# Performance work log

Hardware: AMD Instinct MI355X
Metric: run time of the kernel (lower is better)

The kernel has to match this reference:

```python
import jax, jax.numpy as jnp
import numpy as np

TAU = 0.1
EPS = 1e-8  # torch CosineSimilarity eps


def _neg_indices(B):
    # static (numpy) column indices of the non-masked (negative) entries per row
    N = 2 * B
    mask = ~(np.eye(N, dtype=bool)
             | np.eye(N, k=B, dtype=bool)
             | np.eye(N, k=-B, dtype=bool))
    return np.where(mask)[1].reshape(N, N - 2)  # [2B, 2B-2]


def setup_inputs() -> dict:
    key = jax.random.key(0)
    k1, k2 = jax.random.split(key)
    zis = jax.random.normal(k1, (4096, 128), dtype=jnp.float32)
    zjs = jax.random.normal(k2, (4096, 128), dtype=jnp.float32)
    return {"zis": zis, "zjs": zjs}


def reference(zis, zjs):
    B = zis.shape[0]
    N = 2 * B
    reps = jnp.concatenate([zjs, zis], axis=0)  # [2B, D]
    # cosine similarity via normalize + GEMM
    norm = jnp.linalg.norm(reps, axis=-1, keepdims=True)
    rn = reps / jnp.maximum(norm, EPS)
    sim = rn @ rn.T  # [2B, 2B]

    l_pos = jnp.diagonal(sim, offset=B)   # [B]
    r_pos = jnp.diagonal(sim, offset=-B)  # [B]
    positives = jnp.concatenate([l_pos, r_pos])[:, None]  # [2B, 1]

    neg_idx = jnp.asarray(_neg_indices(B))  # static [2B, 2B-2]
    negatives = jnp.take_along_axis(sim, neg_idx, axis=1)  # [2B, 2B-2]

    logits = jnp.concatenate([positives, negatives], axis=1) / TAU  # [2B, 2B-1]
    logp = jax.nn.log_softmax(logits, axis=-1)
    # labels are all zeros; CrossEntropyLoss(reduction='sum')
    CE = -jnp.sum(logp[:, 0])
    # pt = mean over full [2B, 2B-1] of onehot * softmax = sum softmax[:,0] / (2B*(2B-1))
    pt = jnp.sum(jnp.exp(logp[:, 0])) / (N * (N - 1))
    epsilon = float(B)
    loss = CE / N + epsilon * (1.0 / B - pt)
    return loss
```

## Files before the change

kernel.cpp:

```cpp
#include <hip/hip_runtime.h>
#include <hip/hip_bf16.h>

#define BSZ 4096
#define NSZ 8192
#define DD  128
#define TILE 128
#define GROUPS 8
#define TPB 8

typedef __attribute__((ext_vector_type(8))) short bf16x8;
typedef __attribute__((ext_vector_type(4))) float f32x4;

typedef __attribute__((address_space(3))) unsigned int lds_u32;
typedef const __attribute__((address_space(1))) unsigned int glb_u32;

__global__ __launch_bounds__(256)
void norm_kernel(const float* __restrict__ zis,
                 const float* __restrict__ zjs,
                 __hip_bfloat16* __restrict__ rn) {
    const int row  = blockIdx.x * 4 + (threadIdx.x >> 6);
    const int lane = threadIdx.x & 63;
    const float* src = (row < BSZ) ? (zjs + (size_t)row * DD)
                                   : (zis + (size_t)(row - BSZ) * DD);
    float2 v = *(const float2*)(src + lane * 2);
    float ss = v.x * v.x + v.y * v.y;
    #pragma unroll
    for (int off = 32; off; off >>= 1) ss += __shfl_xor(ss, off);
    float inv = 1.0f / fmaxf(sqrtf(ss), 1e-8f);
    __hip_bfloat16 a = __float2bfloat16(v.x * inv);
    __hip_bfloat16 b = __float2bfloat16(v.y * inv);
    ushort2 pk;
    pk.x = *(const ushort*)&a;
    pk.y = *(const ushort*)&b;
    *(ushort2*)(rn + (size_t)row * DD + lane * 2) = pk;
}

__global__ __launch_bounds__(512)
void sim_lse_kernel(const __hip_bfloat16* __restrict__ rn,
                    float* __restrict__ partials,
                    float* __restrict__ pos) {
    __shared__ ushort Bt[2][TILE * DD];

    const int g   = blockIdx.x;
    const int bi  = blockIdx.y;
    const int tid = threadIdx.x;
    const int wid  = tid >> 6;
    const int lane = tid & 63;
    const int l15  = lane & 15;
    const int kg   = lane >> 4;
    const int wm   = wid >> 1;
    const int wn   = wid & 1;

    const char* abase = (const char*)rn + (size_t)(bi * TILE + wm * 32 + l15) * 256;
    bf16x8 af[2][4];
    #pragma unroll
    for (int mf = 0; mf < 2; ++mf)
        #pragma unroll
        for (int kk = 0; kk < 4; ++kk)
            af[mf][kk] = *(const bf16x8*)(abase + mf * 16 * 256 + kk * 64 + kg * 16);

    {
        const char* gbase = (const char*)rn + (size_t)(g * TPB) * TILE * 256;
        #pragma unroll
        for (int j = 0; j < 4; ++j) {
            int cs  = (wid * 4 + j) * 64 + lane;
            int gsc = cs ^ ((cs >> 4) & 7);
            __builtin_amdgcn_global_load_lds((glb_u32*)(gbase + (size_t)gsc * 16),
                                             (lds_u32*)(&Bt[0][0] + (wid * 4 + j) * 512),
                                             16, 0, 0);
        }
    }
    __syncthreads();

    float rsum[2][4] = {};
    const int bjp = (bi + 32) & 63;
    const int nfd = (wm & 1) * 2;
    const bool wdiag = (wn == (wm >> 1));

    for (int t = 0; t < TPB; ++t) {
        const int bj = g * TPB + t;

        if (t + 1 < TPB) {
            const char* gbase = (const char*)rn + (size_t)(bj + 1) * TILE * 256;
            ushort* dst = &Bt[(t + 1) & 1][0];
            #pragma unroll
            for (int j = 0; j < 4; ++j) {
                int cs  = (wid * 4 + j) * 64 + lane;
                int gsc = cs ^ ((cs >> 4) & 7);
                __builtin_amdgcn_global_load_lds((glb_u32*)(gbase + (size_t)gsc * 16),
                                                 (lds_u32*)(dst + (wid * 4 + j) * 512),
                                                 16, 0, 0);
            }
        }

        f32x4 acc[2][4] = {};
        const char* Bb = (const char*)&Bt[t & 1][0];
        #pragma unroll
        for (int kk = 0; kk < 4; ++kk) {
            const int kb = kk * 64 + kg * 16;
            bf16x8 bfr[4];
            #pragma unroll
            for (int nf = 0; nf < 4; ++nf) {
                int cR = wn * 64 + nf * 16 + l15;
                int o = cR * 256 + kb;
                bfr[nf] = *(const bf16x8*)(Bb + (o ^ ((cR & 7) << 4)));
            }
            #pragma unroll
            for (int mf = 0; mf < 2; ++mf)
                #pragma unroll
                for (int nf = 0; nf < 4; ++nf)
                    acc[mf][nf] = __builtin_amdgcn_mfma_f32_16x16x32_bf16(
                        af[mf][kk], bfr[nf], acc[mf][nf], 0, 0, 0);
        }

        const bool dglb = (bj == bi)  && wdiag;
        const bool pglb = (bj == bjp) && wdiag;
        #pragma unroll
        for (int mf = 0; mf < 2; ++mf) {
            #pragma unroll
            for (int nf = 0; nf < 4; ++nf) {
                #pragma unroll
                for (int reg = 0; reg < 4; ++reg) {
                    float s = acc[mf][nf][reg];
                    bool hit = (nf == nfd + mf) && (kg * 4 + reg == l15);
                    if (pglb && hit)
                        pos[bi * TILE + wm * 32 + mf * 16 + l15] = s;
                    float p = __expf(s * 10.0f);
                    if (dglb && hit) p = 0.0f;
                    rsum[mf][reg] += p;
                }
            }
        }

        __syncthreads();
    }

    #pragma unroll
    for (int mf = 0; mf < 2; ++mf)
        #pragma unroll
        for (int reg = 0; reg < 4; ++reg) {
            float v = rsum[mf][reg];
            v += __shfl_xor(v, 1);
            v += __shfl_xor(v, 2);
            v += __shfl_xor(v, 4);
            v += __shfl_xor(v, 8);
            if (l15 == 0)
                partials[(size_t)(g * 2 + wn) * NSZ
                         + bi * TILE + wm * 32 + mf * 16 + kg * 4 + reg] = v;
        }
}

__global__ __launch_bounds__(1024)
void reduce_kernel(const float* __restrict__ partials,
                   const float* __restrict__ pos,
                   float* __restrict__ out) {
    int tid = threadIdx.x;
    int base = tid * 8;
    float se[8] = {0.f, 0.f, 0.f, 0.f, 0.f, 0.f, 0.f, 0.f};
    #pragma unroll
    for (int gr = 0; gr < 2 * GROUPS; ++gr) {
        const float* p = partials + (size_t)gr * NSZ + base;
        float4 a = *(const float4*)(p);
        float4 b = *(const float4*)(p + 4);
        se[0] += a.x; se[1] += a.y; se[2] += a.z; se[3] += a.w;
        se[4] += b.x; se[5] += b.y; se[6] += b.z; se[7] += b.w;
    }
    float ce = 0.f, pt = 0.f;
    #pragma unroll
    for (int h = 0; h < 2; ++h) {
        float4 p4 = *(const float4*)(pos + base + h * 4);
        const float* pp = (const float*)&p4;
        #pragma unroll
        for (int q = 0; q < 4; ++q) {
            float s = se[h * 4 + q];
            ce += __logf(s) - pp[q] * 10.0f;
            pt += __expf(pp[q] * 10.0f) / s;
        }
    }
    #pragma unroll
    for (int off = 32; off; off >>= 1) {
        ce += __shfl_xor(ce, off);
        pt += __shfl_xor(pt, off);
    }
    __shared__ float lce[16], lpt[16];
    if ((tid & 63) == 0) { lce[tid >> 6] = ce; lpt[tid >> 6] = pt; }
    __syncthreads();
    if (tid == 0) {
        float CE = 0.f, PT = 0.f;
        #pragma unroll
        for (int w = 0; w < 16; ++w) { CE += lce[w]; PT += lpt[w]; }
        float loss = CE / (float)NSZ + 1.0f
                   - PT * ((float)BSZ / ((float)NSZ * (float)(NSZ - 1)));
        out[0] = loss;
    }
}

extern "C" void kernel_launch(void* const* d_in, const int* in_sizes, int n_in,
                              void* d_out, int out_size, void* d_ws, size_t ws_size,
                              hipStream_t stream) {
    const float* zis = (const float*)d_in[0];
    const float* zjs = (const float*)d_in[1];
    float* out = (float*)d_out;

    char* ws = (char*)d_ws;
    __hip_bfloat16* rn = (__hip_bfloat16*)ws;
    float* partials = (float*)(ws + 2 * 1024 * 1024);
    float* pos      = (float*)(ws + 2 * 1024 * 1024 + 512 * 1024);

    norm_kernel<<<NSZ / 4, 256, 0, stream>>>(zis, zjs, rn);

    dim3 grid(GROUPS, 64);
    sim_lse_kernel<<<grid, 512, 0, stream>>>(rn, partials, pos);

    reduce_kernel<<<1, 1024, 0, stream>>>(partials, pos, out);
}
```

Before: 46.22 us.

## Stage A tile in LDS and single-buffer B to raise occupancy

The A fragments were held in registers for the whole kernel. They are now staged once into LDS and re-read every iteration. The B double buffer is replaced with a single buffer that is loaded after compute, with a second barrier per tile. A launch-bounds occupancy hint of 4 is added. The aim is to cut register pressure and allow more resident blocks, at the cost of extra LDS reads and losing the overlap of the global load with compute.

```diff
diff --git a/kernel.cpp b/kernel.cpp
--- a/kernel.cpp
+++ b/kernel.cpp
@@ -35,11 +35,12 @@
     *(ushort2*)(rn + (size_t)row * DD + lane * 2) = pk;
 }
 
-__global__ __launch_bounds__(512)
+__global__ __launch_bounds__(512, 4)
 void sim_lse_kernel(const __hip_bfloat16* __restrict__ rn,
                     float* __restrict__ partials,
                     float* __restrict__ pos) {
-    __shared__ ushort Bt[2][TILE * DD];
+    __shared__ ushort As[TILE * DD];
+    __shared__ ushort Bs[TILE * DD];
 
     const int g   = blockIdx.x;
     const int bi  = blockIdx.y;
@@ -51,22 +52,18 @@
     const int wm   = wid >> 1;
     const int wn   = wid & 1;
 
-    const char* abase = (const char*)rn + (size_t)(bi * TILE + wm * 32 + l15) * 256;
-    bf16x8 af[2][4];
-    #pragma unroll
-    for (int mf = 0; mf < 2; ++mf)
-        #pragma unroll
-        for (int kk = 0; kk < 4; ++kk)
-            af[mf][kk] = *(const bf16x8*)(abase + mf * 16 * 256 + kk * 64 + kg * 16);
-
     {
-        const char* gbase = (const char*)rn + (size_t)(g * TPB) * TILE * 256;
+        const char* ga = (const char*)rn + (size_t)bi * TILE * 256;
+        const char* gb = (const char*)rn + (size_t)(g * TPB) * TILE * 256;
         #pragma unroll
         for (int j = 0; j < 4; ++j) {
             int cs  = (wid * 4 + j) * 64 + lane;
             int gsc = cs ^ ((cs >> 4) & 7);
-            __builtin_amdgcn_global_load_lds((glb_u32*)(gbase + (size_t)gsc * 16),
-                                             (lds_u32*)(&Bt[0][0] + (wid * 4 + j) * 512),
+            __builtin_amdgcn_global_load_lds((glb_u32*)(ga + (size_t)gsc * 16),
+                                             (lds_u32*)(As + (wid * 4 + j) * 512),
+                                             16, 0, 0);
+            __builtin_amdgcn_global_load_lds((glb_u32*)(gb + (size_t)gsc * 16),
+                                             (lds_u32*)(Bs + (wid * 4 + j) * 512),
                                              16, 0, 0);
         }
     }
@@ -76,28 +73,23 @@
     const int bjp = (bi + 32) & 63;
     const int nfd = (wm & 1) * 2;
     const bool wdiag = (wn == (wm >> 1));
+    const char* Ab = (const char*)As;
+    const char* Bb = (const char*)Bs;
 
     for (int t = 0; t < TPB; ++t) {
         const int bj = g * TPB + t;
 
-        if (t + 1 < TPB) {
-            const char* gbase = (const char*)rn + (size_t)(bj + 1) * TILE * 256;
-            ushort* dst = &Bt[(t + 1) & 1][0];
-            #pragma unroll
-            for (int j = 0; j < 4; ++j) {
-                int cs  = (wid * 4 + j) * 64 + lane;
-                int gsc = cs ^ ((cs >> 4) & 7);
-                __builtin_amdgcn_global_load_lds((glb_u32*)(gbase + (size_t)gsc * 16),
-                                                 (lds_u32*)(dst + (wid * 4 + j) * 512),
-                                                 16, 0, 0);
-            }
-        }
-
         f32x4 acc[2][4] = {};
-        const char* Bb = (const char*)&Bt[t & 1][0];
         #pragma unroll
         for (int kk = 0; kk < 4; ++kk) {
             const int kb = kk * 64 + kg * 16;
+            bf16x8 afr[2];
+            #pragma unroll
+            for (int mf = 0; mf < 2; ++mf) {
+                int rR = wm * 32 + mf * 16 + l15;
+                int o = rR * 256 + kb;
+                afr[mf] = *(const bf16x8*)(Ab + (o ^ ((rR & 7) << 4)));
+            }
             bf16x8 bfr[4];
             #pragma unroll
             for (int nf = 0; nf < 4; ++nf) {
@@ -110,7 +102,7 @@
                 #pragma unroll
                 for (int nf = 0; nf < 4; ++nf)
                     acc[mf][nf] = __builtin_amdgcn_mfma_f32_16x16x32_bf16(
-                        af[mf][kk], bfr[nf], acc[mf][nf], 0, 0, 0);
+                        afr[mf], bfr[nf], acc[mf][nf], 0, 0, 0);
         }
 
         const bool dglb = (bj == bi)  && wdiag;
@@ -133,6 +125,19 @@
         }
 
         __syncthreads();
+
+        if (t + 1 < TPB) {
+            const char* gb = (const char*)rn + (size_t)(bj + 1) * TILE * 256;
+            #pragma unroll
+            for (int j = 0; j < 4; ++j) {
+                int cs  = (wid * 4 + j) * 64 + lane;
+                int gsc = cs ^ ((cs >> 4) & 7);
+                __builtin_amdgcn_global_load_lds((glb_u32*)(gb + (size_t)gsc * 16),
+                                                 (lds_u32*)(Bs + (wid * 4 + j) * 512),
+                                                 16, 0, 0);
+            }
+            __syncthreads();
+        }
     }
 
     #pragma unroll
```

Measured after the change: 41.74 us. 9.7% less time.
